# Performance work log

Hardware: AMD Instinct MI355X
Metric: run time of the kernel (lower is better)

## Reference

```python
import jax, jax.numpy as jnp
import numpy as np

B, D, H, E, K = 8192, 1024, 4096, 8, 2


def setup_inputs() -> dict:
    key = jax.random.key(0)
    ks = jax.random.split(key, 7)
    s = 0.02
    return {
        "x": jax.random.normal(ks[0], (B, D), dtype=jnp.float32),
        "Wr": jax.random.normal(ks[1], (D, E), dtype=jnp.float32) * s,
        "br": jnp.zeros((E,), dtype=jnp.float32),
        "W1": jax.random.normal(ks[2], (E, D, H), dtype=jnp.float32) * s,
        "b1": jnp.zeros((E, H), dtype=jnp.float32),
        "W2": jax.random.normal(ks[3], (E, H, D), dtype=jnp.float32) * s,
        "b2": jnp.zeros((E, D), dtype=jnp.float32),
    }


def reference(x, Wr, br, W1, b1, W2, b2):
    # Router (eval mode: no noise, no dropout)
    logits = x @ Wr + br                              # [B, E]
    probs = jax.nn.softmax(logits, axis=-1)
    top_w, top_i = jax.lax.top_k(probs, K)            # [B, K]
    top_w = top_w / jnp.sum(top_w, axis=-1, keepdims=True)
    # Sparse combine weights as a dense [B, E] matrix (only K nonzeros per row)
    rows = jnp.arange(x.shape[0])[:, None]
    combine = jnp.zeros_like(probs).at[rows, top_i].add(top_w)  # [B, E]
    # Per-expert MLP over all tokens (dense dispatch), exact erf GELU as torch
    h = jax.nn.gelu(jnp.einsum('bd,edh->ebh', x, W1) + b1[:, None, :],
                    approximate=False)                # [E, B, H]
    y = jnp.einsum('ebh,eho->ebo', h, W2) + b2[:, None, :]  # [E, B, D]
    # Weighted scatter-combine
    out = jnp.einsum('be,ebo->bo', combine, y)        # [B, D]
    return out
```

## Files before the change

kernel.cpp:

```cpp
#include <hip/hip_runtime.h>
#include <hip/hip_bf16.h>
#include <cstdint>
#include <cstddef>

#define B_TOK 8192
#define DIM   1024
#define HID   4096
#define NEXP  8
#define MAXSLOT 17408

typedef __bf16 bf16x8 __attribute__((ext_vector_type(8)));
typedef float  f32x4  __attribute__((ext_vector_type(4)));

__device__ __forceinline__ void load_lds16(const void* g, void* l) {
  __builtin_amdgcn_global_load_lds(
      (const __attribute__((address_space(1))) void*)g,
      (__attribute__((address_space(3))) void*)l, 16, 0, 0);
}

__device__ __forceinline__ uint16_t f2b(float f) {
  uint32_t u = __builtin_bit_cast(uint32_t, f);
  return (uint16_t)((u + 0x7FFFu + ((u >> 16) & 1u)) >> 16);
}
__device__ __forceinline__ float b2f(uint32_t hbits) {
  uint32_t u = hbits << 16;
  return __builtin_bit_cast(float, u);
}

__global__ void init_kernel(int* __restrict__ rows16k, int* __restrict__ counts,
                            int* __restrict__ cursor, float* __restrict__ zeropad) {
  int i = blockIdx.x * 256 + threadIdx.x;
  if (i < MAXSLOT) rows16k[i] = -1;
  if (i < NEXP) { counts[i] = 0; cursor[i] = 0; }
  if (i < 16) zeropad[i] = 0.f;
}

__global__ void transpose_cvt2_kernel(const float* __restrict__ W1, uint16_t* __restrict__ W1b,
                                      const float* __restrict__ W2, uint16_t* __restrict__ W2b) {
  const int which = blockIdx.z >> 3, e = blockIdx.z & 7;
  const int M = which ? HID : DIM;
  const int N = which ? DIM : HID;
  if (blockIdx.x * 64 >= N || blockIdx.y * 64 >= M) return;
  const float* in = (which ? W2 : W1) + (size_t)e * M * N;
  uint16_t* out = (which ? W2b : W1b) + (size_t)e * M * N;

  __shared__ uint16_t tile[64][66];
  const int t = threadIdx.x;
  const int lr = t & 15, lw = t >> 4;

#pragma unroll
  for (int i = 0; i < 4; i++) {
    const int ml = lw + i * 16;
    const int nl = lr * 4;
    float4 v = *(const float4*)(in + (size_t)(blockIdx.y * 64 + ml) * N + blockIdx.x * 64 + nl);
    uint64_t p = (uint64_t)f2b(v.x) | ((uint64_t)f2b(v.y) << 16) |
                 ((uint64_t)f2b(v.z) << 32) | ((uint64_t)f2b(v.w) << 48);
    *(uint64_t*)&tile[ml][nl] = p;
  }
  __syncthreads();
#pragma unroll
  for (int i = 0; i < 4; i++) {
    const int nl = lw + i * 16;
    const int ml = lr * 4;
    uint64_t p = (uint64_t)tile[ml + 0][nl] | ((uint64_t)tile[ml + 1][nl] << 16) |
                 ((uint64_t)tile[ml + 2][nl] << 32) | ((uint64_t)tile[ml + 3][nl] << 48);
    *(uint64_t*)(out + (size_t)(blockIdx.x * 64 + nl) * M + blockIdx.y * 64 + ml) = p;
  }
}

__global__ void router_kernel(const float* __restrict__ x, const float* __restrict__ Wr,
                              const float* __restrict__ br, int* __restrict__ top_i,
                              float* __restrict__ top_w, uint16_t* __restrict__ xb) {
  const int wave = threadIdx.x >> 6, lane = threadIdx.x & 63;
  const int b = blockIdx.x * 4 + wave;
  const float* xr = x + (size_t)b * DIM;
  uint16_t* xbr = xb + (size_t)b * DIM;
  float acc[NEXP];
#pragma unroll
  for (int e = 0; e < NEXP; e++) acc[e] = 0.f;
#pragma unroll
  for (int i = 0; i < 4; i++) {
    const int d0 = i * 256 + lane * 4;
    float4 xv = *(const float4*)(xr + d0);
    uint64_t p = (uint64_t)f2b(xv.x) | ((uint64_t)f2b(xv.y) << 16) |
                 ((uint64_t)f2b(xv.z) << 32) | ((uint64_t)f2b(xv.w) << 48);
    *(uint64_t*)(xbr + d0) = p;
    float xs[4] = {xv.x, xv.y, xv.z, xv.w};
#pragma unroll
    for (int j = 0; j < 4; j++) {
      const float4* wr = (const float4*)(Wr + (size_t)(d0 + j) * NEXP);
      float4 w0 = wr[0], w1 = wr[1];
      acc[0] += xs[j] * w0.x; acc[1] += xs[j] * w0.y;
      acc[2] += xs[j] * w0.z; acc[3] += xs[j] * w0.w;
      acc[4] += xs[j] * w1.x; acc[5] += xs[j] * w1.y;
      acc[6] += xs[j] * w1.z; acc[7] += xs[j] * w1.w;
    }
  }
#pragma unroll
  for (int e = 0; e < NEXP; e++)
#pragma unroll
    for (int off = 32; off; off >>= 1) acc[e] += __shfl_xor(acc[e], off);
  if (lane == 0) {
    float l[NEXP];
#pragma unroll
    for (int e = 0; e < NEXP; e++) l[e] = acc[e] + br[e];
    int i0 = 0; float v0 = l[0];
#pragma unroll
    for (int e = 1; e < NEXP; e++) if (l[e] > v0) { v0 = l[e]; i0 = e; }
    int i1 = -1; float v1 = -3.4e38f;
#pragma unroll
    for (int e = 0; e < NEXP; e++) if (e != i0 && l[e] > v1) { v1 = l[e]; i1 = e; }
    float w0 = 1.f / (1.f + expf(v1 - v0));
    float w1 = 1.f - w0;
    top_i[b * 2 + 0] = i0; top_i[b * 2 + 1] = i1;
    top_w[b * 2 + 0] = w0; top_w[b * 2 + 1] = w1;
  }
}

__global__ void count_kernel(const int* __restrict__ top_i, int* __restrict__ counts) {
  const int b = blockIdx.x * 256 + threadIdx.x;
  const int lane = threadIdx.x & 63;
#pragma unroll
  for (int k = 0; k < 2; k++) {
    const int e = top_i[b * 2 + k];
#pragma unroll
    for (int ex = 0; ex < NEXP; ex++) {
      unsigned long long m = __ballot(e == ex);
      if (e == ex) {
        int leader = __ffsll((long long)m) - 1;
        if (lane == leader) atomicAdd(&counts[ex], __popcll(m));
      }
    }
  }
}

__global__ void offsets_kernel(const int* __restrict__ counts, int* __restrict__ off_p) {
  int o = 0;
  for (int e = 0; e < NEXP; e++) { off_p[e] = o; o += (counts[e] + 127) & ~127; }
  off_p[NEXP] = o;
}

__global__ void scatter_kernel(const int* __restrict__ top_i, const float* __restrict__ top_w,
                               const int* __restrict__ off_p, int* __restrict__ cursor,
                               int* __restrict__ rows16k, float* __restrict__ wgt,
                               int* __restrict__ slot_of) {
  const int b = blockIdx.x * 256 + threadIdx.x;
  const int lane = threadIdx.x & 63;
#pragma unroll
  for (int k = 0; k < 2; k++) {
    const int e = top_i[b * 2 + k];
    const float w = top_w[b * 2 + k];
    int pos = 0;
#pragma unroll
    for (int ex = 0; ex < NEXP; ex++) {
      unsigned long long m = __ballot(e == ex);
      if (e == ex) {
        int nset = __popcll(m);
        int rank = __popcll(m & ((1ull << lane) - 1ull));
        int leader = __ffsll((long long)m) - 1;
        int base = 0;
        if (lane == leader) base = atomicAdd(&cursor[ex], nset);
        base = __shfl(base, leader);
        pos = off_p[ex] + base + rank;
      }
    }
    rows16k[pos] = b;
    wgt[pos] = w;
    slot_of[b * 2 + k] = pos;
  }
}

template<bool GATHER, bool GELU>
__global__ __launch_bounds__(256, 4) void gemm128_kernel(
    const uint16_t* __restrict__ Abase, const uint16_t* __restrict__ Wb,
    const float* __restrict__ bias, const int* __restrict__ rows16k,
    const int* __restrict__ counts, const int* __restrict__ off_p,
    const float* __restrict__ zeropad, uint16_t* __restrict__ outb,
    int Nfull, int Kdim) {
  const int e = blockIdx.x;
  const int ne = counts[e];
  const int rb = blockIdx.z;
  if (rb * 128 >= ne) return;
  const int nbase = blockIdx.y * 128;
  const int sbase = off_p[e] + rb * 128;
  const int nt = Kdim / 64;

  __shared__ __align__(16) uint16_t smem[2 * 128 * 64];

  const int tid = threadIdx.x;
  const int lane = tid & 63;
  const int wid = tid >> 6;
  const int wm = wid >> 1, wn = wid & 1;
  const int lr = lane & 15, lh = lane >> 4;
  const int swz8 = (((tid & 7) ^ ((tid >> 3) & 7)) * 8);

  const uint16_t* srcA[4]; int stA[4];
  const uint16_t* srcB[4];
#pragma unroll
  for (int is = 0; is < 4; is++) {
    const int r = (tid >> 3) + is * 32;
    if (GATHER) {
      int tok = rows16k[sbase + r];
      srcA[is] = (tok >= 0) ? (Abase + (size_t)tok * Kdim + swz8) : (const uint16_t*)zeropad;
      stA[is] = (tok >= 0) ? 64 : 0;
    } else {
      srcA[is] = Abase + (size_t)(sbase + r) * Kdim + swz8;
      stA[is] = 64;
    }
    srcB[is] = Wb + ((size_t)e * Nfull + nbase + r) * Kdim + swz8;
  }

  f32x4 acc[4][4];
#pragma unroll
  for (int mi = 0; mi < 4; mi++)
#pragma unroll
    for (int ni = 0; ni < 4; ni++) acc[mi][ni] = (f32x4){0.f, 0.f, 0.f, 0.f};

  for (int t = 0; t < nt; ++t) {
    uint16_t* dA = &smem[0];
    uint16_t* dB = dA + 8192;
#pragma unroll
    for (int is = 0; is < 4; is++) {
      load_lds16(srcA[is], dA + (is * 256 + tid) * 8);
      load_lds16(srcB[is], dB + (is * 256 + tid) * 8);
      srcA[is] += stA[is]; srcB[is] += 64;
    }
    __syncthreads();

#pragma unroll
    for (int kk = 0; kk < 2; kk++) {
      bf16x8 afr[4], bfr[4];
#pragma unroll
      for (int ni = 0; ni < 4; ni++) {
        const int row = wn * 64 + ni * 16 + lr;
        const int c = (kk * 4 + lh) ^ (lr & 7);
        bfr[ni] = *(const bf16x8*)&dB[row * 64 + c * 8];
      }
#pragma unroll
      for (int mi = 0; mi < 4; mi++) {
        const int row = wm * 64 + mi * 16 + lr;
        const int c = (kk * 4 + lh) ^ (lr & 7);
        afr[mi] = *(const bf16x8*)&dA[row * 64 + c * 8];
      }
      __builtin_amdgcn_s_setprio(1);
#pragma unroll
      for (int mi = 0; mi < 4; mi++)
#pragma unroll
        for (int ni = 0; ni < 4; ni++)
          acc[mi][ni] = __builtin_amdgcn_mfma_f32_16x16x32_bf16(afr[mi], bfr[ni], acc[mi][ni], 0, 0, 0);
      __builtin_amdgcn_s_setprio(0);
    }
    __syncthreads();
  }

  float biasv[4];
#pragma unroll
  for (int ni = 0; ni < 4; ni++)
    biasv[ni] = bias[(size_t)e * Nfull + nbase + wn * 64 + ni * 16 + lr];
#pragma unroll
  for (int mi = 0; mi < 4; mi++)
#pragma unroll
    for (int ni = 0; ni < 4; ni++)
#pragma unroll
      for (int r = 0; r < 4; r++) {
        const int row = wm * 64 + mi * 16 + lh * 4 + r;
        const int col = nbase + wn * 64 + ni * 16 + lr;
        float t = acc[mi][ni][r] + biasv[ni];
        float g;
        if (GELU) {
          float t2 = t * t;
          float v = t * fmaf(0.1029437f, t2, 2.3022085f);
          float ex = exp2f(v);
          float rr = 1.0f / (ex + 1.0f);
          g = t - t * rr;
        } else {
          g = t;
        }
        outb[(size_t)(sbase + row) * Nfull + col] = f2b(g);
      }
}

__global__ void combine_kernel(const uint16_t* __restrict__ y, const int* __restrict__ slot_of,
                               const float* __restrict__ top_w, float* __restrict__ out) {
  const int b = blockIdx.x;
  const int t = threadIdx.x;
  const int s0 = slot_of[b * 2], s1 = slot_of[b * 2 + 1];
  const float w0 = top_w[b * 2], w1 = top_w[b * 2 + 1];
  uint64_t p0 = *(const uint64_t*)(y + (size_t)s0 * DIM + t * 4);
  uint64_t p1 = *(const uint64_t*)(y + (size_t)s1 * DIM + t * 4);
  float4 r;
  r.x = w0 * b2f((uint32_t)(p0 >> 0) & 0xFFFFu)  + w1 * b2f((uint32_t)(p1 >> 0) & 0xFFFFu);
  r.y = w0 * b2f((uint32_t)(p0 >> 16) & 0xFFFFu) + w1 * b2f((uint32_t)(p1 >> 16) & 0xFFFFu);
  r.z = w0 * b2f((uint32_t)(p0 >> 32) & 0xFFFFu) + w1 * b2f((uint32_t)(p1 >> 32) & 0xFFFFu);
  r.w = w0 * b2f((uint32_t)(p0 >> 48) & 0xFFFFu) + w1 * b2f((uint32_t)(p1 >> 48) & 0xFFFFu);
  *(float4*)(out + (size_t)b * DIM + t * 4) = r;
}

extern "C" void kernel_launch(void* const* d_in, const int* in_sizes, int n_in,
                              void* d_out, int out_size, void* d_ws, size_t ws_size,
                              hipStream_t stream) {
  const float* x  = (const float*)d_in[0];
  const float* Wr = (const float*)d_in[1];
  const float* br = (const float*)d_in[2];
  const float* W1 = (const float*)d_in[3];
  const float* b1 = (const float*)d_in[4];
  const float* W2 = (const float*)d_in[5];
  const float* b2 = (const float*)d_in[6];
  float* out = (float*)d_out;

  char* ws = (char*)d_ws;
  uint16_t* W1b = (uint16_t*)ws; ws += (size_t)NEXP * HID * DIM * 2;
  uint16_t* W2b = (uint16_t*)ws; ws += (size_t)NEXP * DIM * HID * 2;
  uint16_t* xb  = (uint16_t*)ws; ws += (size_t)B_TOK * DIM * 2;
  uint16_t* h   = (uint16_t*)ws; ws += (size_t)MAXSLOT * HID * 2;
  uint16_t* yb  = (uint16_t*)ws; ws += (size_t)MAXSLOT * DIM * 2;
  int*   top_i  = (int*)ws;   ws += (size_t)B_TOK * 2 * 4;
  float* top_w  = (float*)ws; ws += (size_t)B_TOK * 2 * 4;
  int*   slot_of= (int*)ws;   ws += (size_t)B_TOK * 2 * 4;
  int*   rows16k= (int*)ws;   ws += (size_t)MAXSLOT * 4;
  float* wgt    = (float*)ws; ws += (size_t)MAXSLOT * 4;
  int*   counts = (int*)ws;   ws += 64;
  int*   cursor = (int*)ws;   ws += 64;
  int*   off_p  = (int*)ws;   ws += 64;
  float* zeropad= (float*)ws; ws += 64;

  init_kernel<<<dim3((MAXSLOT + 255) / 256), dim3(256), 0, stream>>>(rows16k, counts, cursor, zeropad);
  transpose_cvt2_kernel<<<dim3(64, 64, 16), dim3(256), 0, stream>>>(W1, W1b, W2, W2b);
  router_kernel<<<dim3(B_TOK / 4), dim3(256), 0, stream>>>(x, Wr, br, top_i, top_w, xb);
  count_kernel<<<dim3(B_TOK / 256), dim3(256), 0, stream>>>(top_i, counts);
  offsets_kernel<<<dim3(1), dim3(1), 0, stream>>>(counts, off_p);
  scatter_kernel<<<dim3(B_TOK / 256), dim3(256), 0, stream>>>(top_i, top_w, off_p, cursor, rows16k, wgt, slot_of);
  gemm128_kernel<true, true><<<dim3(NEXP, HID / 128, MAXSLOT / 128), dim3(256), 0, stream>>>(
      xb, W1b, b1, rows16k, counts, off_p, zeropad, h, HID, DIM);
  gemm128_kernel<false, false><<<dim3(NEXP, DIM / 128, MAXSLOT / 128), dim3(256), 0, stream>>>(
      h, W2b, b2, rows16k, counts, off_p, zeropad, yb, DIM, HID);
  combine_kernel<<<dim3(B_TOK), dim3(256), 0, stream>>>(yb, slot_of, top_w, out);
}
```

Measured before the change: 549.1 us.

## Double-buffer LDS tiles with K-step 32 and prefetch next tile before compute

Replaces the single-buffered K=64 LDS tile with two K=32 buffers in the same LDS footprint. The next tile is issued via global_load_lds before computing the current one, with a manual vmcnt wait and raw barriers, so global loads overlap the MFMA work. The LDS layout is also remapped: each 64-element row now packs two 32-wide halves from rows r and r+64, with a new XOR swizzle. The cost is twice as many barriers and iterations per K, and correctness depends on the exact vmcnt count and the compiler not reordering memory ops.

```diff
diff --git a/kernel.cpp b/kernel.cpp
--- a/kernel.cpp
+++ b/kernel.cpp
@@ -183,31 +183,34 @@
   if (rb * 128 >= ne) return;
   const int nbase = blockIdx.y * 128;
   const int sbase = off_p[e] + rb * 128;
-  const int nt = Kdim / 64;
-
-  __shared__ __align__(16) uint16_t smem[2 * 128 * 64];
+  const int nt = Kdim / 32;
+
+  __shared__ __align__(16) uint16_t smem[2 * 8192];
 
   const int tid = threadIdx.x;
   const int lane = tid & 63;
   const int wid = tid >> 6;
   const int wm = wid >> 1, wn = wid & 1;
   const int lr = lane & 15, lh = lane >> 4;
-  const int swz8 = (((tid & 7) ^ ((tid >> 3) & 7)) * 8);
-
-  const uint16_t* srcA[4]; int stA[4];
-  const uint16_t* srcB[4];
-#pragma unroll
-  for (int is = 0; is < 4; is++) {
-    const int r = (tid >> 3) + is * 32;
+
+  const uint16_t* srcA[2]; int stA[2];
+  const uint16_t* srcB[2];
+#pragma unroll
+  for (int is = 0; is < 2; is++) {
+    const int idx = is * 256 + tid;
+    const int lrow = idx >> 3;
+    const int j0 = (idx & 7) ^ (lrow & 7);
+    const int r = lrow + 64 * (j0 >> 2);
+    const int c = (j0 & 3) * 8;
     if (GATHER) {
       int tok = rows16k[sbase + r];
-      srcA[is] = (tok >= 0) ? (Abase + (size_t)tok * Kdim + swz8) : (const uint16_t*)zeropad;
-      stA[is] = (tok >= 0) ? 64 : 0;
+      srcA[is] = (tok >= 0) ? (Abase + (size_t)tok * Kdim + c) : (const uint16_t*)zeropad;
+      stA[is] = (tok >= 0) ? 32 : 0;
     } else {
-      srcA[is] = Abase + (size_t)(sbase + r) * Kdim + swz8;
-      stA[is] = 64;
-    }
-    srcB[is] = Wb + ((size_t)e * Nfull + nbase + r) * Kdim + swz8;
+      srcA[is] = Abase + (size_t)(sbase + r) * Kdim + c;
+      stA[is] = 32;
+    }
+    srcB[is] = Wb + ((size_t)e * Nfull + nbase + r) * Kdim + c;
   }
 
   f32x4 acc[4][4];
@@ -216,41 +219,48 @@
 #pragma unroll
     for (int ni = 0; ni < 4; ni++) acc[mi][ni] = (f32x4){0.f, 0.f, 0.f, 0.f};
 
+  const int jA = ((wm << 2) | lh) ^ (lr & 7);
+  const int jB = ((wn << 2) | lh) ^ (lr & 7);
+
+  auto STAGE = [&](int buf) {
+    uint16_t* dA = &smem[buf * 8192];
+    uint16_t* dB = dA + 4096;
+    load_lds16(srcA[0], dA + tid * 8);
+    load_lds16(srcA[1], dA + (256 + tid) * 8);
+    load_lds16(srcB[0], dB + tid * 8);
+    load_lds16(srcB[1], dB + (256 + tid) * 8);
+    srcA[0] += stA[0]; srcA[1] += stA[1]; srcB[0] += 32; srcB[1] += 32;
+  };
+
+  STAGE(0);
+
   for (int t = 0; t < nt; ++t) {
-    uint16_t* dA = &smem[0];
-    uint16_t* dB = dA + 8192;
-#pragma unroll
-    for (int is = 0; is < 4; is++) {
-      load_lds16(srcA[is], dA + (is * 256 + tid) * 8);
-      load_lds16(srcB[is], dB + (is * 256 + tid) * 8);
-      srcA[is] += stA[is]; srcB[is] += 64;
-    }
-    __syncthreads();
-
-#pragma unroll
-    for (int kk = 0; kk < 2; kk++) {
-      bf16x8 afr[4], bfr[4];
-#pragma unroll
-      for (int ni = 0; ni < 4; ni++) {
-        const int row = wn * 64 + ni * 16 + lr;
-        const int c = (kk * 4 + lh) ^ (lr & 7);
-        bfr[ni] = *(const bf16x8*)&dB[row * 64 + c * 8];
-      }
-#pragma unroll
-      for (int mi = 0; mi < 4; mi++) {
-        const int row = wm * 64 + mi * 16 + lr;
-        const int c = (kk * 4 + lh) ^ (lr & 7);
-        afr[mi] = *(const bf16x8*)&dA[row * 64 + c * 8];
-      }
-      __builtin_amdgcn_s_setprio(1);
-#pragma unroll
-      for (int mi = 0; mi < 4; mi++)
-#pragma unroll
-        for (int ni = 0; ni < 4; ni++)
-          acc[mi][ni] = __builtin_amdgcn_mfma_f32_16x16x32_bf16(afr[mi], bfr[ni], acc[mi][ni], 0, 0, 0);
-      __builtin_amdgcn_s_setprio(0);
-    }
-    __syncthreads();
+    const int cb = t & 1;
+    if (t + 1 < nt) {
+      STAGE(cb ^ 1);
+      asm volatile("s_waitcnt vmcnt(4)" ::: "memory");
+    } else {
+      asm volatile("s_waitcnt vmcnt(0)" ::: "memory");
+    }
+    __builtin_amdgcn_s_barrier();
+
+    const uint16_t* sA = &smem[cb * 8192];
+    const uint16_t* sB = sA + 4096;
+    bf16x8 afr[4], bfr[4];
+#pragma unroll
+    for (int mi = 0; mi < 4; mi++)
+      afr[mi] = *(const bf16x8*)&sA[(mi * 16 + lr) * 64 + jA * 8];
+#pragma unroll
+    for (int ni = 0; ni < 4; ni++)
+      bfr[ni] = *(const bf16x8*)&sB[(ni * 16 + lr) * 64 + jB * 8];
+    __builtin_amdgcn_s_setprio(1);
+#pragma unroll
+    for (int mi = 0; mi < 4; mi++)
+#pragma unroll
+      for (int ni = 0; ni < 4; ni++)
+        acc[mi][ni] = __builtin_amdgcn_mfma_f32_16x16x32_bf16(afr[mi], bfr[ni], acc[mi][ni], 0, 0, 0);
+    __builtin_amdgcn_s_setprio(0);
+    __builtin_amdgcn_s_barrier();
   }
 
   float biasv[4];
```

Result: slower. 578.9 us (+5.4%).

## Enlarge expert GEMM block tile to 256x128 with 512 threads

Applied to the files above, without the earlier changes.

The grouped expert GEMMs now use a 256-row by 128-column block tile computed by eight waves instead of a 128x128 tile with four waves. Each weight tile loaded into LDS is therefore reused across twice as many token rows, which cuts weight traffic and block count. The global-to-LDS load mapping and swizzle are recomputed for the larger block. Per-expert slot padding rises to 256 rows, adding some wasted rows, and LDS use per block grows.

```diff
diff --git a/kernel.cpp b/kernel.cpp
--- a/kernel.cpp
+++ b/kernel.cpp
@@ -7,7 +7,7 @@
 #define DIM   1024
 #define HID   4096
 #define NEXP  8
-#define MAXSLOT 17408
+#define MAXSLOT 18432
 
 typedef __bf16 bf16x8 __attribute__((ext_vector_type(8)));
 typedef float  f32x4  __attribute__((ext_vector_type(4)));
@@ -136,7 +136,7 @@
 
 __global__ void offsets_kernel(const int* __restrict__ counts, int* __restrict__ off_p) {
   int o = 0;
-  for (int e = 0; e < NEXP; e++) { off_p[e] = o; o += (counts[e] + 127) & ~127; }
+  for (int e = 0; e < NEXP; e++) { off_p[e] = o; o += (counts[e] + 255) & ~255; }
   off_p[NEXP] = o;
 }
 
@@ -171,7 +171,7 @@
 }
 
 template<bool GATHER, bool GELU>
-__global__ __launch_bounds__(256, 4) void gemm128_kernel(
+__global__ __launch_bounds__(512, 2) void gemm256x128_kernel(
     const uint16_t* __restrict__ Abase, const uint16_t* __restrict__ Wb,
     const float* __restrict__ bias, const int* __restrict__ rows16k,
     const int* __restrict__ counts, const int* __restrict__ off_p,
@@ -180,34 +180,41 @@
   const int e = blockIdx.x;
   const int ne = counts[e];
   const int rb = blockIdx.z;
-  if (rb * 128 >= ne) return;
+  if (rb * 256 >= ne) return;
   const int nbase = blockIdx.y * 128;
-  const int sbase = off_p[e] + rb * 128;
+  const int sbase = off_p[e] + rb * 256;
   const int nt = Kdim / 64;
 
-  __shared__ __align__(16) uint16_t smem[2 * 128 * 64];
+  __shared__ __align__(16) uint16_t smem[(256 + 128) * 64];
 
   const int tid = threadIdx.x;
   const int lane = tid & 63;
   const int wid = tid >> 6;
   const int wm = wid >> 1, wn = wid & 1;
   const int lr = lane & 15, lh = lane >> 4;
-  const int swz8 = (((tid & 7) ^ ((tid >> 3) & 7)) * 8);
 
   const uint16_t* srcA[4]; int stA[4];
-  const uint16_t* srcB[4];
+  const uint16_t* srcB[2];
 #pragma unroll
   for (int is = 0; is < 4; is++) {
-    const int r = (tid >> 3) + is * 32;
+    const int idx = is * 512 + tid;
+    const int r = idx >> 3;
+    const int j0 = (idx & 7) ^ (r & 7);
     if (GATHER) {
       int tok = rows16k[sbase + r];
-      srcA[is] = (tok >= 0) ? (Abase + (size_t)tok * Kdim + swz8) : (const uint16_t*)zeropad;
+      srcA[is] = (tok >= 0) ? (Abase + (size_t)tok * Kdim + j0 * 8) : (const uint16_t*)zeropad;
       stA[is] = (tok >= 0) ? 64 : 0;
     } else {
-      srcA[is] = Abase + (size_t)(sbase + r) * Kdim + swz8;
+      srcA[is] = Abase + (size_t)(sbase + r) * Kdim + j0 * 8;
       stA[is] = 64;
     }
-    srcB[is] = Wb + ((size_t)e * Nfull + nbase + r) * Kdim + swz8;
+  }
+#pragma unroll
+  for (int is = 0; is < 2; is++) {
+    const int idx = is * 512 + tid;
+    const int r = idx >> 3;
+    const int j0 = (idx & 7) ^ (r & 7);
+    srcB[is] = Wb + ((size_t)e * Nfull + nbase + r) * Kdim + j0 * 8;
   }
 
   f32x4 acc[4][4];
@@ -216,14 +223,19 @@
 #pragma unroll
     for (int ni = 0; ni < 4; ni++) acc[mi][ni] = (f32x4){0.f, 0.f, 0.f, 0.f};
 
+  uint16_t* dA = &smem[0];
+  uint16_t* dB = dA + 256 * 64;
+
   for (int t = 0; t < nt; ++t) {
-    uint16_t* dA = &smem[0];
-    uint16_t* dB = dA + 8192;
 #pragma unroll
     for (int is = 0; is < 4; is++) {
-      load_lds16(srcA[is], dA + (is * 256 + tid) * 8);
-      load_lds16(srcB[is], dB + (is * 256 + tid) * 8);
-      srcA[is] += stA[is]; srcB[is] += 64;
+      load_lds16(srcA[is], dA + (is * 512 + tid) * 8);
+      srcA[is] += stA[is];
+    }
+#pragma unroll
+    for (int is = 0; is < 2; is++) {
+      load_lds16(srcB[is], dB + (is * 512 + tid) * 8);
+      srcB[is] += 64;
     }
     __syncthreads();
 
@@ -330,9 +342,9 @@
   count_kernel<<<dim3(B_TOK / 256), dim3(256), 0, stream>>>(top_i, counts);
   offsets_kernel<<<dim3(1), dim3(1), 0, stream>>>(counts, off_p);
   scatter_kernel<<<dim3(B_TOK / 256), dim3(256), 0, stream>>>(top_i, top_w, off_p, cursor, rows16k, wgt, slot_of);
-  gemm128_kernel<true, true><<<dim3(NEXP, HID / 128, MAXSLOT / 128), dim3(256), 0, stream>>>(
+  gemm256x128_kernel<true, true><<<dim3(NEXP, HID / 128, MAXSLOT / 256), dim3(512), 0, stream>>>(
       xb, W1b, b1, rows16k, counts, off_p, zeropad, h, HID, DIM);
-  gemm128_kernel<false, false><<<dim3(NEXP, DIM / 128, MAXSLOT / 128), dim3(256), 0, stream>>>(
+  gemm256x128_kernel<false, false><<<dim3(NEXP, DIM / 128, MAXSLOT / 256), dim3(512), 0, stream>>>(
       h, W2b, b2, rows16k, counts, off_p, zeropad, yb, DIM, HID);
   combine_kernel<<<dim3(B_TOK), dim3(256), 0, stream>>>(yb, slot_of, top_w, out);
 }
```

Measured after the change: 692.1 us. 1.26x slower.
